# Kernel optimization log

Hardware: AMD Instinct MI355X
Metric: run time of the kernel (lower is better)

## Reference

```python
import jax, jax.numpy as jnp
import numpy as np

ITERS = 3
LAMB = 0.05
EPS = 1e-6


def _l2norm(x):
    return x / jnp.clip(jnp.linalg.norm(x, axis=-1, keepdims=True), 1e-8)


def setup_inputs() -> dict:
    key = jax.random.key(0)
    k1, k2, k3, k4 = jax.random.split(key, 4)
    bi, bt, R, W, D = 128, 128, 36, 50, 256
    imgs = jax.random.normal(k1, (bi, R, D), dtype=jnp.float32)
    caps = jax.random.normal(k2, (bt, W, D), dtype=jnp.float32)
    # valid lengths in [1, max]; pin element 0 to max so int(lens.max()) == static dim
    img_lens = jax.random.randint(k3, (bi,), 1, R + 1).at[0].set(R)
    cap_lens = jax.random.randint(k4, (bt,), 1, W + 1).at[0].set(W)
    return {"imgs": imgs, "caps": caps, "img_lens": img_lens, "cap_lens": cap_lens}


def _forward(imgs, caps, img_lens, cap_lens):
    bi, R, D = imgs.shape
    bt, W, _ = caps.shape
    # fine-grained cosine similarities: [bi, bt, R, W]
    fg_sims = jnp.einsum("ird,jwd->ijrw", _l2norm(imgs), _l2norm(caps))
    # mask[i,j,r,w] = (r < img_lens[i]) & (w < cap_lens[j])
    rmask = jnp.arange(R) < img_lens[:, None]          # [bi, R]
    wmask = jnp.arange(W) < cap_lens[:, None]          # [bt, W]
    mask = rmask[:, None, :, None] & wmask[None, :, None, :]  # [bi, bt, R, W]
    maskf = mask.astype(fg_sims.dtype)

    # _ave_init: uniform marginals over valid rows / cols
    r = (mask.sum(axis=-1) != 0).astype(fg_sims.dtype)  # [bi, bt, R]
    r = r / r.sum(axis=-1, keepdims=True)
    c = (mask.sum(axis=-2) != 0).astype(fg_sims.dtype)  # [bi, bt, W]
    c = c / c.sum(axis=-1, keepdims=True)

    # Sinkhorn-Knopp on cost (1 - sims); masked entries get cost=INF -> P=0
    P = jnp.where(mask, jnp.exp(-(1.0 - fg_sims) / LAMB), 0.0)
    P = P / (P.sum(axis=(-2, -1), keepdims=True) + EPS)

    def body(P, _):
        u = P.sum(axis=-1) + EPS          # [bi, bt, R]
        P = P * (r / u)[..., :, None]
        v = P.sum(axis=-2) + EPS          # [bi, bt, W]
        P = P * (c / v)[..., None, :]
        return P, None

    P, _ = jax.lax.scan(body, P, None, length=ITERS)
    sims = (fg_sims * P * maskf).sum(axis=(-2, -1))     # [bi, bt]
    return sims


def reference(imgs, caps, img_lens, cap_lens):
    return _forward(imgs, caps, img_lens, cap_lens)
```

## Files before the change

### kernel.cpp

```cpp
#include <hip/hip_runtime.h>
#include <math.h>

#define BI 128
#define BT 128
#define RR 36
#define WW 50
#define DD 256
#define EPSF 1e-6f
#define EXP2_C1 28.85390081777927f
#define EXP2_C0 (-28.85390081777927f)

#define A_TILES 3
#define B_TILES 4
#define KSTEPS 8
#define A_SLOTS (BI * A_TILES * KSTEPS * 64)
#define B_SLOTS (BT * B_TILES * KSTEPS * 64)

#define CV_AT (BI * A_TILES)
#define CV_BT (BT * B_TILES)

typedef short     v8ss __attribute__((ext_vector_type(8)));
typedef _Float16  v8hf __attribute__((ext_vector_type(8)));
typedef float     v4f  __attribute__((ext_vector_type(4)));

template <typename V>
__device__ __forceinline__ auto mfma_impl(V a, V b, v4f c, int)
    -> decltype(__builtin_amdgcn_mfma_f32_16x16x32_f16(a, b, c, 0, 0, 0)) {
    return __builtin_amdgcn_mfma_f32_16x16x32_f16(a, b, c, 0, 0, 0);
}
template <typename V>
__device__ __forceinline__ v4f mfma_impl(V a, V b, v4f c, long) {
    v8ss a2 = __builtin_bit_cast(v8ss, a);
    v8ss b2 = __builtin_bit_cast(v8ss, b);
    return __builtin_amdgcn_mfma_f32_16x16x32_f16(a2, b2, c, 0, 0, 0);
}
__device__ __forceinline__ v4f mfma_f16(v8hf a, v8hf b, v4f c) {
    return mfma_impl(a, b, c, 0);
}

__device__ __forceinline__ float fast_rcp(float x) {
    return __builtin_amdgcn_rcpf(x);
}
__device__ __forceinline__ float fast_exp2(float x) {
    return __builtin_amdgcn_exp2f(x);
}

template <int N>
__device__ __forceinline__ float dpp_ror_add(float x) {
    int xi = __builtin_bit_cast(int, x);
    int yi = __builtin_amdgcn_update_dpp(xi, xi, 0x120 | N, 0xF, 0xF, false);
    return x + __builtin_bit_cast(float, yi);
}
__device__ __forceinline__ float dpp_sum16(float x) {
    x = dpp_ror_add<1>(x);
    x = dpp_ror_add<2>(x);
    x = dpp_ror_add<4>(x);
    x = dpp_ror_add<8>(x);
    return x;
}

__global__ __launch_bounds__(256) void convert_kernel(
    const float* __restrict__ imgs, const float* __restrict__ caps,
    v8ss* __restrict__ Ah_g, v8ss* __restrict__ Bh_g)
{
    __shared__ float raw[16][260];
    __shared__ float invn[16];

    const int t = threadIdx.x;
    const int b = blockIdx.x;
    const bool isA = b < CV_AT;
    int grp, tile, nrows;
    const float* src;
    if (isA) {
        grp = b / A_TILES; tile = b - grp * A_TILES;
        src = imgs + (size_t)grp * RR * DD;
        nrows = RR;
    } else {
        int bb = b - CV_AT;
        grp = bb / B_TILES; tile = bb - grp * B_TILES;
        src = caps + (size_t)grp * WW * DD;
        nrows = WW;
    }
    const size_t tbase = isA ? (size_t)b * (KSTEPS * 64)
                             : (size_t)(b - CV_AT) * (KSTEPS * 64);
    const int r0 = tile << 4;

    for (int f = t; f < 1024; f += 256) {
        const int row = f >> 6, c4 = f & 63;
        float4 v = make_float4(0.f, 0.f, 0.f, 0.f);
        const int r = r0 + row;
        if (r < nrows) v = *(const float4*)(src + (size_t)r * DD + c4 * 4);
        *(float4*)&raw[row][c4 * 4] = v;
    }
    __syncthreads();

    {
        const int row = t >> 4, seg = t & 15;
        float ss = 0.f;
#pragma unroll
        for (int k = 0; k < 16; ++k) {
            float x = raw[row][k * 16 + seg];
            ss += x * x;
        }
        ss = dpp_sum16(ss);
        if (seg == 0) invn[row] = 1.0f / fmaxf(sqrtf(ss), 1e-8f);
    }
    __syncthreads();

    for (int u = t; u < KSTEPS * 64; u += 256) {
        const int ks = u >> 6, sl = u & 63;
        const int rr = sl & 15, kq = sl >> 4;
        const float inv = invn[rr];
        const float* p = &raw[rr][ks * 32 + kq * 8];
        float4 f0 = *(const float4*)p;
        float4 f1 = *(const float4*)(p + 4);
        float xs[8] = {f0.x, f0.y, f0.z, f0.w, f1.x, f1.y, f1.z, f1.w};
        v8hf h;
#pragma unroll
        for (int e = 0; e < 8; ++e) h[e] = (_Float16)(xs[e] * inv);
        if (isA) Ah_g[tbase + (size_t)ks * 64 + sl] = __builtin_bit_cast(v8ss, h);
        else     Bh_g[tbase + (size_t)ks * 64 + sl] = __builtin_bit_cast(v8ss, h);
    }
}

template <int MA, int NA>
__device__ __forceinline__ void pair_body(
    const v8ss* __restrict__ Ah_b, const v8ss* __restrict__ Bh_b,
    const int nr, const int nc, const int lane, float* __restrict__ outp)
{
    v4f acc[MA][NA];
#pragma unroll
    for (int m = 0; m < MA; ++m)
#pragma unroll
        for (int n = 0; n < NA; ++n) acc[m][n] = (v4f){0.f, 0.f, 0.f, 0.f};

    v8hf ah[2][MA], bh[2][NA];
    auto load_stage = [&](int ks, int buf) {
#pragma unroll
        for (int m = 0; m < MA; ++m)
            ah[buf][m] = __builtin_bit_cast(v8hf, Ah_b[(m * KSTEPS + ks) * 64]);
#pragma unroll
        for (int n = 0; n < NA; ++n)
            bh[buf][n] = __builtin_bit_cast(v8hf, Bh_b[(n * KSTEPS + ks) * 64]);
    };

    load_stage(0, 0);
#pragma unroll
    for (int ks = 0; ks < KSTEPS; ++ks) {
        const int cur = ks & 1;
        if (ks + 1 < KSTEPS) load_stage(ks + 1, cur ^ 1);
#pragma unroll
        for (int n = 0; n < NA; ++n)
#pragma unroll
            for (int m = 0; m < MA; ++m)
                acc[m][n] = mfma_f16(ah[cur][m], bh[cur][n], acc[m][n]);
    }

    const int cl = lane & 15;
    const int rq = (lane >> 4) << 2;
    const float inv_nr = 1.0f / (float)nr;
    const float inv_nc = 1.0f / (float)nc;

    float P0[MA][NA][4];
    float tot = 0.f;
#pragma unroll
    for (int m = 0; m < MA; ++m)
#pragma unroll
        for (int n = 0; n < NA; ++n)
#pragma unroll
            for (int q = 0; q < 4; ++q) {
                const int row = (m << 4) + rq + q;
                const int col = (n << 4) + cl;
                float pv = 0.f;
                if (row < nr && col < nc)
                    pv = fast_exp2(fmaf(acc[m][n][q], EXP2_C1, EXP2_C0));
                P0[m][n][q] = pv;
                tot += pv;
            }
    tot = dpp_sum16(tot);
    tot += __shfl_xor(tot, 16, 64);
    tot += __shfl_xor(tot, 32, 64);
    const float gsc = fast_rcp(tot + EPSF);

    float u[MA][4], v[NA];
#pragma unroll
    for (int m = 0; m < MA; ++m)
#pragma unroll
        for (int q = 0; q < 4; ++q) u[m][q] = gsc;
#pragma unroll
    for (int n = 0; n < NA; ++n) v[n] = 1.0f;

#pragma unroll
    for (int it = 0; it < 3; ++it) {
#pragma unroll
        for (int m = 0; m < MA; ++m)
#pragma unroll
            for (int q = 0; q < 4; ++q) {
                float d = 0.f;
#pragma unroll
                for (int n = 0; n < NA; ++n)
                    d = fmaf(P0[m][n][q], v[n], d);
                d = dpp_sum16(d);
                const float t = fmaf(u[m][q], d, EPSF);
                u[m][q] *= inv_nr * fast_rcp(t);
            }
#pragma unroll
        for (int n = 0; n < NA; ++n) {
            float e = 0.f;
#pragma unroll
            for (int m = 0; m < MA; ++m)
#pragma unroll
                for (int q = 0; q < 4; ++q)
                    e = fmaf(P0[m][n][q], u[m][q], e);
            e += __shfl_xor(e, 16, 64);
            e += __shfl_xor(e, 32, 64);
            const float t = fmaf(v[n], e, EPSF);
            v[n] *= inv_nc * fast_rcp(t);
        }
    }

    float osum = 0.f;
#pragma unroll
    for (int m = 0; m < MA; ++m)
#pragma unroll
        for (int n = 0; n < NA; ++n)
#pragma unroll
            for (int q = 0; q < 4; ++q)
                osum = fmaf(acc[m][n][q], P0[m][n][q] * u[m][q] * v[n], osum);
    osum = dpp_sum16(osum);
    osum += __shfl_xor(osum, 16, 64);
    osum += __shfl_xor(osum, 32, 64);
    if (lane == 0) *outp = osum;
}

__global__ __launch_bounds__(64, 4) void pair_kernel(
    const v8ss* __restrict__ Ah_g, const v8ss* __restrict__ Bh_g,
    const int* __restrict__ img_lens, const int* __restrict__ cap_lens,
    float* __restrict__ out)
{
    const int lane = threadIdx.x;
    const int x    = blockIdx.x & 7;
    const int g    = blockIdx.x >> 3;
    const int i    = g >> 4;
    const int j    = (x << 4) + (g & 15);

    const int nr = img_lens[i];
    const int nc = cap_lens[j];
    const int Ma = (nr + 15) >> 4;
    const int Na = (nc + 15) >> 4;

    const v8ss* Ah_b = Ah_g + (size_t)i * (A_TILES * KSTEPS * 64) + lane;
    const v8ss* Bh_b = Bh_g + (size_t)j * (B_TILES * KSTEPS * 64) + lane;
    float* outp = out + i * BT + j;

    const int code = ((Ma - 1) << 2) | (Na - 1);
    switch (code) {
        case 0:  pair_body<1, 1>(Ah_b, Bh_b, nr, nc, lane, outp); break;
        case 1:  pair_body<1, 2>(Ah_b, Bh_b, nr, nc, lane, outp); break;
        case 2:  pair_body<1, 3>(Ah_b, Bh_b, nr, nc, lane, outp); break;
        case 3:  pair_body<1, 4>(Ah_b, Bh_b, nr, nc, lane, outp); break;
        case 4:  pair_body<2, 1>(Ah_b, Bh_b, nr, nc, lane, outp); break;
        case 5:  pair_body<2, 2>(Ah_b, Bh_b, nr, nc, lane, outp); break;
        case 6:  pair_body<2, 3>(Ah_b, Bh_b, nr, nc, lane, outp); break;
        case 7:  pair_body<2, 4>(Ah_b, Bh_b, nr, nc, lane, outp); break;
        case 8:  pair_body<3, 1>(Ah_b, Bh_b, nr, nc, lane, outp); break;
        case 9:  pair_body<3, 2>(Ah_b, Bh_b, nr, nc, lane, outp); break;
        case 10: pair_body<3, 3>(Ah_b, Bh_b, nr, nc, lane, outp); break;
        default: pair_body<3, 4>(Ah_b, Bh_b, nr, nc, lane, outp); break;
    }
}

extern "C" void kernel_launch(void* const* d_in, const int* in_sizes, int n_in,
                              void* d_out, int out_size, void* d_ws, size_t ws_size,
                              hipStream_t stream) {
    const float* imgs     = (const float*)d_in[0];
    const float* caps     = (const float*)d_in[1];
    const int*   img_lens = (const int*)d_in[2];
    const int*   cap_lens = (const int*)d_in[3];
    float* out = (float*)d_out;

    v8ss* Ah_g = (v8ss*)d_ws;
    v8ss* Bh_g = Ah_g + A_SLOTS;

    hipLaunchKernelGGL(convert_kernel, dim3(CV_AT + CV_BT), dim3(256), 0, stream,
                       imgs, caps, Ah_g, Bh_g);
    hipLaunchKernelGGL(pair_kernel, dim3(BI * BT), dim3(64), 0, stream,
                       Ah_g, Bh_g, img_lens, cap_lens, out);
}
```

Baseline: 99.05 us.

## Process two caption pairs per wave, sharing image fragments across fused MFMA loop

Each 64-lane block now handles two (image, caption) pairs that share the same image. When the combined caption tile count fits (Na0+Na1<=4), a single K loop loads the image fragments once and runs MFMAs for both captions, then runs the Sinkhorn epilogue twice. Otherwise it falls back to processing the two pairs one after the other. The grid is halved. This aims to cut redundant A loads and per-block overhead, but it doubles the work per block, raises register pressure, and reduces the number of blocks available for latency hiding.

Measured after the change: 104.1 us. 1.05x slower.

```diff
diff --git a/kernel.cpp b/kernel.cpp
--- a/kernel.cpp
+++ b/kernel.cpp
@@ -124,38 +124,10 @@
 }
 
 template <int MA, int NA>
-__device__ __forceinline__ void pair_body(
-    const v8ss* __restrict__ Ah_b, const v8ss* __restrict__ Bh_b,
-    const int nr, const int nc, const int lane, float* __restrict__ outp)
-{
-    v4f acc[MA][NA];
-#pragma unroll
-    for (int m = 0; m < MA; ++m)
-#pragma unroll
-        for (int n = 0; n < NA; ++n) acc[m][n] = (v4f){0.f, 0.f, 0.f, 0.f};
-
-    v8hf ah[2][MA], bh[2][NA];
-    auto load_stage = [&](int ks, int buf) {
-#pragma unroll
-        for (int m = 0; m < MA; ++m)
-            ah[buf][m] = __builtin_bit_cast(v8hf, Ah_b[(m * KSTEPS + ks) * 64]);
-#pragma unroll
-        for (int n = 0; n < NA; ++n)
-            bh[buf][n] = __builtin_bit_cast(v8hf, Bh_b[(n * KSTEPS + ks) * 64]);
-    };
-
-    load_stage(0, 0);
-#pragma unroll
-    for (int ks = 0; ks < KSTEPS; ++ks) {
-        const int cur = ks & 1;
-        if (ks + 1 < KSTEPS) load_stage(ks + 1, cur ^ 1);
-#pragma unroll
-        for (int n = 0; n < NA; ++n)
-#pragma unroll
-            for (int m = 0; m < MA; ++m)
-                acc[m][n] = mfma_f16(ah[cur][m], bh[cur][n], acc[m][n]);
-    }
-
+__device__ __forceinline__ void sinkhorn_out(
+    const v4f (&acc)[MA][NA], const int nr, const int nc,
+    const int lane, float* __restrict__ outp)
+{
     const int cl = lane & 15;
     const int rq = (lane >> 4) << 2;
     const float inv_nr = 1.0f / (float)nr;
@@ -233,6 +205,112 @@
     if (lane == 0) *outp = osum;
 }
 
+template <int MA, int NA>
+__device__ __forceinline__ void pair_single(
+    const v8ss* __restrict__ Ah_b, const v8ss* __restrict__ Bh_b,
+    const int nr, const int nc, const int lane, float* __restrict__ outp)
+{
+    v4f acc[MA][NA];
+#pragma unroll
+    for (int m = 0; m < MA; ++m)
+#pragma unroll
+        for (int n = 0; n < NA; ++n) acc[m][n] = (v4f){0.f, 0.f, 0.f, 0.f};
+
+    v8hf ah[2][MA], bh[2][NA];
+    auto load_stage = [&](int ks, int buf) {
+#pragma unroll
+        for (int m = 0; m < MA; ++m)
+            ah[buf][m] = __builtin_bit_cast(v8hf, Ah_b[(m * KSTEPS + ks) * 64]);
+#pragma unroll
+        for (int n = 0; n < NA; ++n)
+            bh[buf][n] = __builtin_bit_cast(v8hf, Bh_b[(n * KSTEPS + ks) * 64]);
+    };
+
+    load_stage(0, 0);
+#pragma unroll
+    for (int ks = 0; ks < KSTEPS; ++ks) {
+        const int cur = ks & 1;
+        if (ks + 1 < KSTEPS) load_stage(ks + 1, cur ^ 1);
+#pragma unroll
+        for (int n = 0; n < NA; ++n)
+#pragma unroll
+            for (int m = 0; m < MA; ++m)
+                acc[m][n] = mfma_f16(ah[cur][m], bh[cur][n], acc[m][n]);
+    }
+    sinkhorn_out<MA, NA>(acc, nr, nc, lane, outp);
+}
+
+template <int MA, int NA0, int NA1>
+__device__ __forceinline__ void pair_fused(
+    const v8ss* __restrict__ Ah_b,
+    const v8ss* __restrict__ B0_b, const v8ss* __restrict__ B1_b,
+    const int nr, const int nc0, const int nc1, const int lane,
+    float* __restrict__ o0, float* __restrict__ o1)
+{
+    v4f acc0[MA][NA0], acc1[MA][NA1];
+#pragma unroll
+    for (int m = 0; m < MA; ++m) {
+#pragma unroll
+        for (int n = 0; n < NA0; ++n) acc0[m][n] = (v4f){0.f, 0.f, 0.f, 0.f};
+#pragma unroll
+        for (int n = 0; n < NA1; ++n) acc1[m][n] = (v4f){0.f, 0.f, 0.f, 0.f};
+    }
+
+    v8hf ah[2][MA], b0[2][NA0], b1[2][NA1];
+    auto load_stage = [&](int ks, int buf) {
+#pragma unroll
+        for (int m = 0; m < MA; ++m)
+            ah[buf][m] = __builtin_bit_cast(v8hf, Ah_b[(m * KSTEPS + ks) * 64]);
+#pragma unroll
+        for (int n = 0; n < NA0; ++n)
+            b0[buf][n] = __builtin_bit_cast(v8hf, B0_b[(n * KSTEPS + ks) * 64]);
+#pragma unroll
+        for (int n = 0; n < NA1; ++n)
+            b1[buf][n] = __builtin_bit_cast(v8hf, B1_b[(n * KSTEPS + ks) * 64]);
+    };
+
+    load_stage(0, 0);
+#pragma unroll
+    for (int ks = 0; ks < KSTEPS; ++ks) {
+        const int cur = ks & 1;
+        if (ks + 1 < KSTEPS) load_stage(ks + 1, cur ^ 1);
+#pragma unroll
+        for (int n = 0; n < NA0; ++n)
+#pragma unroll
+            for (int m = 0; m < MA; ++m)
+                acc0[m][n] = mfma_f16(ah[cur][m], b0[cur][n], acc0[m][n]);
+#pragma unroll
+        for (int n = 0; n < NA1; ++n)
+#pragma unroll
+            for (int m = 0; m < MA; ++m)
+                acc1[m][n] = mfma_f16(ah[cur][m], b1[cur][n], acc1[m][n]);
+    }
+    sinkhorn_out<MA, NA0>(acc0, nr, nc0, lane, o0);
+    sinkhorn_out<MA, NA1>(acc1, nr, nc1, lane, o1);
+}
+
+__device__ __forceinline__ void single_dispatch(
+    const v8ss* __restrict__ Ah_b, const v8ss* __restrict__ Bh_b,
+    const int nr, const int nc, const int lane, float* __restrict__ outp)
+{
+    const int Ma = (nr + 15) >> 4;
+    const int Na = (nc + 15) >> 4;
+    switch (((Ma - 1) << 2) | (Na - 1)) {
+        case 0:  pair_single<1, 1>(Ah_b, Bh_b, nr, nc, lane, outp); break;
+        case 1:  pair_single<1, 2>(Ah_b, Bh_b, nr, nc, lane, outp); break;
+        case 2:  pair_single<1, 3>(Ah_b, Bh_b, nr, nc, lane, outp); break;
+        case 3:  pair_single<1, 4>(Ah_b, Bh_b, nr, nc, lane, outp); break;
+        case 4:  pair_single<2, 1>(Ah_b, Bh_b, nr, nc, lane, outp); break;
+        case 5:  pair_single<2, 2>(Ah_b, Bh_b, nr, nc, lane, outp); break;
+        case 6:  pair_single<2, 3>(Ah_b, Bh_b, nr, nc, lane, outp); break;
+        case 7:  pair_single<2, 4>(Ah_b, Bh_b, nr, nc, lane, outp); break;
+        case 8:  pair_single<3, 1>(Ah_b, Bh_b, nr, nc, lane, outp); break;
+        case 9:  pair_single<3, 2>(Ah_b, Bh_b, nr, nc, lane, outp); break;
+        case 10: pair_single<3, 3>(Ah_b, Bh_b, nr, nc, lane, outp); break;
+        default: pair_single<3, 4>(Ah_b, Bh_b, nr, nc, lane, outp); break;
+    }
+}
+
 __global__ __launch_bounds__(64, 4) void pair_kernel(
     const v8ss* __restrict__ Ah_g, const v8ss* __restrict__ Bh_g,
     const int* __restrict__ img_lens, const int* __restrict__ cap_lens,
@@ -241,32 +319,51 @@
     const int lane = threadIdx.x;
     const int x    = blockIdx.x & 7;
     const int g    = blockIdx.x >> 3;
-    const int i    = g >> 4;
-    const int j    = (x << 4) + (g & 15);
-
-    const int nr = img_lens[i];
-    const int nc = cap_lens[j];
-    const int Ma = (nr + 15) >> 4;
-    const int Na = (nc + 15) >> 4;
+    const int i    = g >> 3;
+    const int j0   = (x << 4) + ((g & 7) << 1);
+    const int j1   = j0 + 1;
+
+    const int nr  = img_lens[i];
+    const int nc0 = cap_lens[j0];
+    const int nc1 = cap_lens[j1];
+    const int Ma  = (nr + 15) >> 4;
+    const int Na0 = (nc0 + 15) >> 4;
+    const int Na1 = (nc1 + 15) >> 4;
 
     const v8ss* Ah_b = Ah_g + (size_t)i * (A_TILES * KSTEPS * 64) + lane;
-    const v8ss* Bh_b = Bh_g + (size_t)j * (B_TILES * KSTEPS * 64) + lane;
-    float* outp = out + i * BT + j;
-
-    const int code = ((Ma - 1) << 2) | (Na - 1);
-    switch (code) {
-        case 0:  pair_body<1, 1>(Ah_b, Bh_b, nr, nc, lane, outp); break;
-        case 1:  pair_body<1, 2>(Ah_b, Bh_b, nr, nc, lane, outp); break;
-        case 2:  pair_body<1, 3>(Ah_b, Bh_b, nr, nc, lane, outp); break;
-        case 3:  pair_body<1, 4>(Ah_b, Bh_b, nr, nc, lane, outp); break;
-        case 4:  pair_body<2, 1>(Ah_b, Bh_b, nr, nc, lane, outp); break;
-        case 5:  pair_body<2, 2>(Ah_b, Bh_b, nr, nc, lane, outp); break;
-        case 6:  pair_body<2, 3>(Ah_b, Bh_b, nr, nc, lane, outp); break;
-        case 7:  pair_body<2, 4>(Ah_b, Bh_b, nr, nc, lane, outp); break;
-        case 8:  pair_body<3, 1>(Ah_b, Bh_b, nr, nc, lane, outp); break;
-        case 9:  pair_body<3, 2>(Ah_b, Bh_b, nr, nc, lane, outp); break;
-        case 10: pair_body<3, 3>(Ah_b, Bh_b, nr, nc, lane, outp); break;
-        default: pair_body<3, 4>(Ah_b, Bh_b, nr, nc, lane, outp); break;
+    const v8ss* B0_b = Bh_g + (size_t)j0 * (B_TILES * KSTEPS * 64) + lane;
+    const v8ss* B1_b = Bh_g + (size_t)j1 * (B_TILES * KSTEPS * 64) + lane;
+    float* o0 = out + i * BT + j0;
+    float* o1 = out + i * BT + j1;
+
+    if (Na0 + Na1 <= 4) {
+        switch ((Ma - 1) * 9 + (Na0 - 1) * 3 + (Na1 - 1)) {
+            case 0:  pair_fused<1, 1, 1>(Ah_b, B0_b, B1_b, nr, nc0, nc1, lane, o0, o1); break;
+            case 1:  pair_fused<1, 1, 2>(Ah_b, B0_b, B1_b, nr, nc0, nc1, lane, o0, o1); break;
+            case 2:  pair_fused<1, 1, 3>(Ah_b, B0_b, B1_b, nr, nc0, nc1, lane, o0, o1); break;
+            case 3:  pair_fused<1, 2, 1>(Ah_b, B0_b, B1_b, nr, nc0, nc1, lane, o0, o1); break;
+            case 4:  pair_fused<1, 2, 2>(Ah_b, B0_b, B1_b, nr, nc0, nc1, lane, o0, o1); break;
+            case 6:  pair_fused<1, 3, 1>(Ah_b, B0_b, B1_b, nr, nc0, nc1, lane, o0, o1); break;
+            case 9:  pair_fused<2, 1, 1>(Ah_b, B0_b, B1_b, nr, nc0, nc1, lane, o0, o1); break;
+            case 10: pair_fused<2, 1, 2>(Ah_b, B0_b, B1_b, nr, nc0, nc1, lane, o0, o1); break;
+            case 11: pair_fused<2, 1, 3>(Ah_b, B0_b, B1_b, nr, nc0, nc1, lane, o0, o1); break;
+            case 12: pair_fused<2, 2, 1>(Ah_b, B0_b, B1_b, nr, nc0, nc1, lane, o0, o1); break;
+            case 13: pair_fused<2, 2, 2>(Ah_b, B0_b, B1_b, nr, nc0, nc1, lane, o0, o1); break;
+            case 15: pair_fused<2, 3, 1>(Ah_b, B0_b, B1_b, nr, nc0, nc1, lane, o0, o1); break;
+            case 18: pair_fused<3, 1, 1>(Ah_b, B0_b, B1_b, nr, nc0, nc1, lane, o0, o1); break;
+            case 19: pair_fused<3, 1, 2>(Ah_b, B0_b, B1_b, nr, nc0, nc1, lane, o0, o1); break;
+            case 20: pair_fused<3, 1, 3>(Ah_b, B0_b, B1_b, nr, nc0, nc1, lane, o0, o1); break;
+            case 21: pair_fused<3, 2, 1>(Ah_b, B0_b, B1_b, nr, nc0, nc1, lane, o0, o1); break;
+            case 22: pair_fused<3, 2, 2>(Ah_b, B0_b, B1_b, nr, nc0, nc1, lane, o0, o1); break;
+            case 24: pair_fused<3, 3, 1>(Ah_b, B0_b, B1_b, nr, nc0, nc1, lane, o0, o1); break;
+            default:
+                single_dispatch(Ah_b, B0_b, nr, nc0, lane, o0);
+                single_dispatch(Ah_b, B1_b, nr, nc1, lane, o1);
+                break;
+        }
+    } else {
+        single_dispatch(Ah_b, B0_b, nr, nc0, lane, o0);
+        single_dispatch(Ah_b, B1_b, nr, nc1, lane, o1);
     }
 }
 
@@ -284,6 +381,6 @@
 
     hipLaunchKernelGGL(convert_kernel, dim3(CV_AT + CV_BT), dim3(256), 0, stream,
                        imgs, caps, Ah_g, Bh_g);
-    hipLaunchKernelGGL(pair_kernel, dim3(BI * BT), dim3(64), 0, stream,
+    hipLaunchKernelGGL(pair_kernel, dim3(BI * BT / 2), dim3(64), 0, stream,
                        Ah_g, Bh_g, img_lens, cap_lens, out);
 }
```
